# Kernel tuning notes

Measured on AMD Instinct MI355X. Metric: run time of the kernel, lower is better.

Reference implementation:

```python
import jax, jax.numpy as jnp
import numpy as np

CHUNK_LEN = 32
N_HEAD = 32
HEAD_SIZE = 64
EPS = 1e-5 * 64.0  # GroupNorm eps = 1e-5 * head_size_divisor**2
PREC_MIN = 0.005   # rwkv_inner precision_min_val clamp for fp32


def rwkv_inner(r, k, v, w, u, kv_state, chunk_len):
    # r,k,v,w: [B,H,L,K]; u: [H,K]; kv_state: [B,H,K,V]
    B, H, L, K = k.shape
    T = chunk_len
    N = L // T
    w = jnp.clip(w, PREC_MIN, None)
    wc_log = jnp.log(w).reshape(B, H, N, T, K)
    wc_cum = jnp.cumsum(wc_log, axis=-2)                      # [B,H,N,T,K]
    shifted = jnp.concatenate([jnp.zeros_like(wc_cum[..., :1, :]), wc_cum[..., :-1, :]], axis=-2)
    ws_log = jnp.sum(wc_log, axis=-2, keepdims=True)          # [B,H,N,1,K]
    w_inter = jnp.exp(ws_log - wc_cum)                        # decay to end of chunk
    w_intra = jnp.exp(wc_cum - wc_log)                        # decay from start of chunk
    rc = r.reshape(B, H, N, T, K)
    kc = k.reshape(B, H, N, T, K)
    vc = v.reshape(B, H, N, T, K)
    # intra-chunk attention, log-space offset at T//2 for numerical stability
    off = shifted[..., T // 2:T // 2 + 1, :]
    r_decay = jnp.exp(shifted - off)
    k_inv_decay = jnp.exp(off - wc_cum)
    a = jnp.einsum('bhntk,bhnsk->bhnts', rc * r_decay, kc * k_inv_decay)
    a = jnp.tril(a, -1)
    diag = jnp.einsum('bhntk,bhntk->bhnt', rc, u[None, :, None, None, :] * kc)
    out = jnp.einsum('bhnts,bhnsv->bhntv', a, vc) + diag[..., None] * vc
    # per-chunk (k*w_inter)^T @ v contributions, then sequential state carry
    wkv = jnp.einsum('bhntk,bhntv->bhnkv', kc * w_inter, vc)  # [B,H,N,K,V]
    ws = jnp.exp(ws_log)[:, :, :, 0, :]                       # [B,H,N,K]

    def step(state, xs):
        ws_i, wkv_i = xs
        new_state = state * ws_i[..., None] + wkv_i
        return new_state, state

    final_state, states = jax.lax.scan(step, kv_state, (jnp.moveaxis(ws, 2, 0), jnp.moveaxis(wkv, 2, 0)))
    states = jnp.moveaxis(states, 0, 2)                       # [B,H,N,K,V]
    out = out + jnp.einsum('bhntk,bhnkv->bhntv', rc * w_intra, states)
    return out.reshape(B, H, L, K), final_state


def _forward(x, shift_state, wkv_state,
             time_maa_x, time_maa_w, time_maa_k, time_maa_v, time_maa_r, time_maa_g,
             time_maa_w1, time_maa_w2, time_decay, time_decay_w1, time_decay_w2,
             time_faaaa, Wr, Wk, Wv, Wg, Wo, gn_w, gn_b):
    B, T, C = x.shape
    H, K = N_HEAD, HEAD_SIZE
    xprev = jnp.concatenate([shift_state[:, None, :], x[:, :-1]], axis=1)
    dx = xprev - x
    # token-shift LoRA mixing
    xxx = jnp.tanh((x + dx * time_maa_x) @ time_maa_w1).reshape(B, T, 5, -1)
    m = jnp.einsum('btfe,fec->fbtc', xxx, time_maa_w2)  # [5,B,T,C]
    mw, mk, mv, mr, mg = m[0], m[1], m[2], m[3], m[4]
    xk = x + dx * (time_maa_k + mk)
    xv = x + dx * (time_maa_v + mv)
    xr = x + dx * (time_maa_r + mr)
    xg = x + dx * (time_maa_g + mg)
    xw = x + dx * (time_maa_w + mw)
    r = (xr @ Wr.T).reshape(B, T, H, K).transpose(0, 2, 1, 3)
    k = (xk @ Wk.T).reshape(B, T, H, K).transpose(0, 2, 1, 3)
    v = (xv @ Wv.T).reshape(B, T, H, K).transpose(0, 2, 1, 3)
    g = jax.nn.silu(xg @ Wg.T)
    w = time_decay.reshape(1, H, 1, K) + (jnp.tanh(xw @ time_decay_w1) @ time_decay_w2).reshape(B, T, H, K).transpose(0, 2, 1, 3)
    w = jnp.exp(-jnp.exp(w))
    out, wkv_out = rwkv_inner(r, k, v, w, time_faaaa, wkv_state, CHUNK_LEN)
    out = out.transpose(0, 2, 1, 3).reshape(B, T, C)
    # GroupNorm with H groups of K channels
    og = out.reshape(B, T, H, K)
    mu = og.mean(-1, keepdims=True)
    var = og.var(-1, keepdims=True)
    og = (og - mu) * jax.lax.rsqrt(var + EPS)
    out = og.reshape(B, T, C) * gn_w + gn_b
    out = (out * g) @ Wo.T
    return out, x[:, -1], wkv_out


def setup_inputs() -> dict:
    B, T, C = 4, 2048, 2048
    H, K = N_HEAD, HEAD_SIZE
    E5, TD = 32, 64
    key = jax.random.key(0)
    ks = jax.random.split(key, 24)
    f32 = jnp.float32
    inp = {
        'x': jax.random.normal(ks[0], (B, T, C), f32),
        'shift_state': jax.random.normal(ks[1], (B, C), f32),
        'wkv_state': jax.random.normal(ks[2], (B, H, K, K), f32) * 0.1,
        'time_maa_x': jax.random.uniform(ks[3], (1, 1, C), f32),
        'time_maa_w': jax.random.uniform(ks[4], (1, 1, C), f32),
        'time_maa_k': jax.random.uniform(ks[5], (1, 1, C), f32),
        'time_maa_v': jax.random.uniform(ks[6], (1, 1, C), f32),
        'time_maa_r': jax.random.uniform(ks[7], (1, 1, C), f32),
        'time_maa_g': jax.random.uniform(ks[8], (1, 1, C), f32),
        'time_maa_w1': jax.random.uniform(ks[9], (C, E5 * 5), f32, -1e-4, 1e-4),
        'time_maa_w2': jax.random.normal(ks[10], (5, E5, C), f32) * 0.01,
        'time_decay': jnp.linspace(-6.0, -1.0, C, dtype=f32).reshape(1, 1, C),
        'time_decay_w1': jax.random.uniform(ks[11], (C, TD), f32, -1e-4, 1e-4),
        'time_decay_w2': jax.random.normal(ks[12], (TD, C), f32) * 0.01,
        'time_faaaa': jax.random.normal(ks[13], (H, K), f32) * 0.1,
        'Wr': jax.random.normal(ks[14], (C, C), f32) * 0.02,
        'Wk': jax.random.normal(ks[15], (C, C), f32) * 0.02,
        'Wv': jax.random.normal(ks[16], (C, C), f32) * 0.02,
        'Wg': jax.random.normal(ks[17], (C, C), f32) * 0.02,
        'Wo': jax.random.normal(ks[18], (C, C), f32) * 0.02,
        'gn_w': jnp.ones((C,), f32),
        'gn_b': jnp.zeros((C,), f32),
    }
    return inp


def reference(x, shift_state, wkv_state,
              time_maa_x, time_maa_w, time_maa_k, time_maa_v, time_maa_r, time_maa_g,
              time_maa_w1, time_maa_w2, time_decay, time_decay_w1, time_decay_w2,
              time_faaaa, Wr, Wk, Wv, Wg, Wo, gn_w, gn_b):
    return _forward(x, shift_state, wkv_state,
                    time_maa_x, time_maa_w, time_maa_k, time_maa_v, time_maa_r, time_maa_g,
                    time_maa_w1, time_maa_w2, time_decay, time_decay_w1, time_decay_w2,
                    time_faaaa, Wr, Wk, Wv, Wg, Wo, gn_w, gn_b)
```

## Files before the change

kernel.cpp:

```cpp
#include <hip/hip_runtime.h>
#include <stdint.h>
#include <math.h>


typedef __attribute__((ext_vector_type(8))) short bf16x8;
typedef __attribute__((ext_vector_type(4))) float f32x4;

#define AS1(p) ((const __attribute__((address_space(1))) void*)(p))
#define AS3(p) ((__attribute__((address_space(3))) void*)(p))

__device__ __forceinline__ unsigned short f2bf(float f) {
  unsigned int u = __builtin_bit_cast(unsigned int, f);
  u += 0x7fffu + ((u >> 16) & 1u);
  return (unsigned short)(u >> 16);
}
__device__ __forceinline__ float bf2f(unsigned short s) {
  unsigned int u = ((unsigned int)s) << 16;
  return __builtin_bit_cast(float, u);
}
__device__ __forceinline__ unsigned int packbf(float lo, float hi) {
  return (unsigned int)f2bf(lo) | ((unsigned int)f2bf(hi) << 16);
}

template <int EPI, bool BOUNDS>
__global__ __launch_bounds__(256) void gemm_nt(
    const unsigned short* __restrict__ A, const unsigned short* __restrict__ B,
    void* __restrict__ Cp, int M, int N, int K, const float* __restrict__ evec,
    int slot)
{
  __shared__ __align__(16) unsigned short As[128 * 32];
  __shared__ __align__(16) unsigned short Bs[128 * 32];
  const int tid = threadIdx.x;
  const int l = tid & 63, w = tid >> 6;
  const int wm = w & 1, wn = w >> 1;
  const int lm = l & 15, quad = l >> 4;
  const long mBase = (long)blockIdx.y * 128;
  const long nBase = (long)blockIdx.x * 128;

  f32x4 acc[4][4];
  f32x4 zero = {0.f, 0.f, 0.f, 0.f};
#pragma unroll
  for (int i = 0; i < 4; i++)
#pragma unroll
    for (int j = 0; j < 4; j++) acc[i][j] = zero;

  for (int k0 = 0; k0 < K; k0 += 32) {
    if (!BOUNDS) {
      const int r0 = w * 32;
      const int lr = l >> 2, lc = l & 3;
      const unsigned short* gA = A + (mBase + r0 + lr) * (long)K + k0 + lc * 8;
      __builtin_amdgcn_global_load_lds(AS1(gA), AS3(&As[r0 * 32]), 16, 0, 0);
      const unsigned short* gA2 = gA + 16 * (long)K;
      __builtin_amdgcn_global_load_lds(AS1(gA2), AS3(&As[(r0 + 16) * 32]), 16, 0, 0);
      const unsigned short* gB = B + (nBase + r0 + lr) * (long)K + k0 + lc * 8;
      __builtin_amdgcn_global_load_lds(AS1(gB), AS3(&Bs[r0 * 32]), 16, 0, 0);
      const unsigned short* gB2 = gB + 16 * (long)K;
      __builtin_amdgcn_global_load_lds(AS1(gB2), AS3(&Bs[(r0 + 16) * 32]), 16, 0, 0);
    } else {
      const int row = tid >> 2, ch = tid & 3;
#pragma unroll
      for (int rr = 0; rr < 128; rr += 64) {
        int r = rr + row;
        *(int4*)&As[r * 32 + ch * 8] =
            *(const int4*)&A[(mBase + r) * (long)K + k0 + ch * 8];
        int4 bv = make_int4(0, 0, 0, 0);
        long nG = nBase + r;
        if (nG < N) bv = *(const int4*)&B[nG * (long)K + k0 + ch * 8];
        *(int4*)&Bs[r * 32 + ch * 8] = bv;
      }
    }
    __syncthreads();
    bf16x8 af[4], bq[4];
#pragma unroll
    for (int i = 0; i < 4; i++)
      af[i] = *(const bf16x8*)&As[(wm * 64 + i * 16 + lm) * 32 + quad * 8];
#pragma unroll
    for (int i = 0; i < 4; i++)
      bq[i] = *(const bf16x8*)&Bs[(wn * 64 + i * 16 + lm) * 32 + quad * 8];
#pragma unroll
    for (int mi = 0; mi < 4; mi++)
#pragma unroll
      for (int ni = 0; ni < 4; ni++)
        acc[mi][ni] = __builtin_amdgcn_mfma_f32_16x16x32_bf16(af[mi], bq[ni], acc[mi][ni], 0, 0, 0);
    __syncthreads();
  }

#pragma unroll
  for (int mi = 0; mi < 4; mi++) {
#pragma unroll
    for (int ni = 0; ni < 4; ni++) {
      long col = nBase + wn * 64 + ni * 16 + lm;
      if (BOUNDS && col >= N) continue;
      long rw0 = mBase + wm * 64 + mi * 16 + quad * 4;
#pragma unroll
      for (int r = 0; r < 4; r++) {
        float y = acc[mi][ni][r];
        long row = rw0 + r;
        long off = row * (long)N + col;
        if constexpr (EPI == 0) {
          ((float*)Cp)[off] = y;
        } else if constexpr (EPI == 2) {
          ((unsigned short*)Cp)[off] = f2bf(tanhf(y));
        } else if constexpr (EPI == 3) {
          ((unsigned short*)Cp)[off] = f2bf(y / (1.f + __expf(-y)));
        } else if constexpr (EPI == 4) {
          float wv = evec[col] + y;
          ((_Float16*)Cp)[off] = (_Float16)fmaxf(-__expf(wv), -5.2983174f);
        } else if constexpr (EPI == 5) {
          int b = (int)(row >> 11), t = (int)(row & 2047);
          int n = t >> 5, tt = t & 31;
          int h = (int)(col >> 6), kk = (int)(col & 63);
          long c = ((long)(b * 32 + h)) * 64 + n;
          ((unsigned short*)Cp)[c * 6144 + slot + tt * 64 + kk] = f2bf(y);
        }
      }
    }
  }
}

template <int EPI>
__global__ __launch_bounds__(512, 1) void gemm256_nt(
    const unsigned short* __restrict__ A, const unsigned short* __restrict__ B,
    void* __restrict__ Cp, int M, int N, int K, int slot)
{
  __shared__ __align__(16) unsigned short As2[2][16384];
  __shared__ __align__(16) unsigned short Bs2[2][16384];
  const int tid = threadIdx.x;
  const int l = tid & 63;
  const int w = tid >> 6;
  const int wm = w >> 2, wn = w & 3;
  const int lm = l & 15, quad = l >> 4;
  const long mBase = (long)blockIdx.y * 256;
  const long nBase = (long)blockIdx.x * 256;
  const int NT = K >> 6;

  const int r0 = tid >> 3;
  const int csw = (tid & 7) ^ (r0 & 7);
  const int ldsOff = (tid & ~63) * 8;
  const unsigned short* ga0 = A + (mBase + r0) * (long)K + csw * 8;
  const unsigned short* gb0 = B + (nBase + r0) * (long)K + csw * 8;

  f32x4 acc[8][4];
  f32x4 zero = {0.f, 0.f, 0.f, 0.f};
#pragma unroll
  for (int i = 0; i < 8; i++)
#pragma unroll
    for (int j = 0; j < 4; j++) acc[i][j] = zero;

#define STAGE256(kt_)                                                          \
  {                                                                            \
    const int _b = (kt_) & 1;                                                  \
    const unsigned short* _ga = ga0 + (long)(kt_) * 64;                        \
    const unsigned short* _gb = gb0 + (long)(kt_) * 64;                        \
    __builtin_amdgcn_global_load_lds(AS1(_ga), AS3(&As2[_b][ldsOff]), 16, 0, 0);              \
    __builtin_amdgcn_global_load_lds(AS1(_gb), AS3(&Bs2[_b][ldsOff]), 16, 0, 0);              \
    __builtin_amdgcn_global_load_lds(AS1(_ga + (long)64 * K), AS3(&As2[_b][4096 + ldsOff]), 16, 0, 0);  \
    __builtin_amdgcn_global_load_lds(AS1(_gb + (long)64 * K), AS3(&Bs2[_b][4096 + ldsOff]), 16, 0, 0);  \
    __builtin_amdgcn_global_load_lds(AS1(_ga + (long)128 * K), AS3(&As2[_b][8192 + ldsOff]), 16, 0, 0); \
    __builtin_amdgcn_global_load_lds(AS1(_gb + (long)128 * K), AS3(&Bs2[_b][8192 + ldsOff]), 16, 0, 0); \
    __builtin_amdgcn_global_load_lds(AS1(_ga + (long)192 * K), AS3(&As2[_b][12288 + ldsOff]), 16, 0, 0);\
    __builtin_amdgcn_global_load_lds(AS1(_gb + (long)192 * K), AS3(&Bs2[_b][12288 + ldsOff]), 16, 0, 0);\
  }

  STAGE256(0);
  STAGE256(1);
  asm volatile("s_waitcnt vmcnt(8)" ::: "memory");
  __builtin_amdgcn_s_barrier();

  const int q0 = (quad ^ (lm & 7)) * 8;
  const int rA = (wm * 128 + lm) * 64;
  const int rB = (wn * 64 + lm) * 64;

  for (int kt = 0; kt < NT; ++kt) {
    const int b = kt & 1;
    bf16x8 af[8][2], bq[4][2];
#pragma unroll
    for (int fm = 0; fm < 8; fm++)
      af[fm][0] = *(const bf16x8*)&As2[b][rA + fm * 1024 + q0];
#pragma unroll
    for (int fn = 0; fn < 4; fn++)
      bq[fn][0] = *(const bf16x8*)&Bs2[b][rB + fn * 1024 + q0];
#pragma unroll
    for (int fm = 0; fm < 8; fm++)
      af[fm][1] = *(const bf16x8*)&As2[b][rA + fm * 1024 + (q0 ^ 32)];
#pragma unroll
    for (int fn = 0; fn < 4; fn++)
      bq[fn][1] = *(const bf16x8*)&Bs2[b][rB + fn * 1024 + (q0 ^ 32)];

    __builtin_amdgcn_s_setprio(1);
#pragma unroll
    for (int fm = 0; fm < 8; fm++)
#pragma unroll
      for (int fn = 0; fn < 4; fn++)
        acc[fm][fn] = __builtin_amdgcn_mfma_f32_16x16x32_bf16(af[fm][0], bq[fn][0], acc[fm][fn], 0, 0, 0);
    __builtin_amdgcn_s_setprio(0);

    asm volatile("s_waitcnt lgkmcnt(0)" ::: "memory");
    __builtin_amdgcn_s_barrier();
    if (kt + 2 < NT) STAGE256(kt + 2);

    __builtin_amdgcn_s_setprio(1);
#pragma unroll
    for (int fm = 0; fm < 8; fm++)
#pragma unroll
      for (int fn = 0; fn < 4; fn++)
        acc[fm][fn] = __builtin_amdgcn_mfma_f32_16x16x32_bf16(af[fm][1], bq[fn][1], acc[fm][fn], 0, 0, 0);
    __builtin_amdgcn_s_setprio(0);

    if (kt + 2 < NT) {
      asm volatile("s_waitcnt vmcnt(8)" ::: "memory");
    } else {
      asm volatile("s_waitcnt vmcnt(0)" ::: "memory");
    }
    __builtin_amdgcn_s_barrier();
  }
#undef STAGE256

#pragma unroll
  for (int mi = 0; mi < 8; mi++) {
#pragma unroll
    for (int ni = 0; ni < 4; ni++) {
      long col = nBase + wn * 64 + ni * 16 + lm;
      long rw0 = mBase + wm * 128 + mi * 16 + quad * 4;
#pragma unroll
      for (int r = 0; r < 4; r++) {
        float y = acc[mi][ni][r];
        long row = rw0 + r;
        long off = row * (long)N + col;
        if constexpr (EPI == 0) {
          ((float*)Cp)[off] = y;
        } else if constexpr (EPI == 3) {
          ((unsigned short*)Cp)[off] = f2bf(y / (1.f + __expf(-y)));
        } else if constexpr (EPI == 5) {
          int bb = (int)(row >> 11), t = (int)(row & 2047);
          int n = t >> 5, tt = t & 31;
          int h = (int)(col >> 6), kk = (int)(col & 63);
          long c = ((long)(bb * 32 + h)) * 64 + n;
          ((unsigned short*)Cp)[c * 6144 + slot + tt * 64 + kk] = f2bf(y);
        }
      }
    }
  }
}

__global__ __launch_bounds__(256) void k_convert(const float* __restrict__ s,
                                                 unsigned short* __restrict__ d, int n4)
{
  int i = blockIdx.x * 256 + threadIdx.x;
  if (i >= n4) return;
  float4 v = ((const float4*)s)[i];
  short4 o;
  o.x = (short)f2bf(v.x); o.y = (short)f2bf(v.y);
  o.z = (short)f2bf(v.z); o.w = (short)f2bf(v.w);
  ((short4*)d)[i] = o;
}

__global__ __launch_bounds__(256) void k_transpose(const float* __restrict__ s,
                                                   unsigned short* __restrict__ d, int R, int C)
{
  int i = blockIdx.x * 256 + threadIdx.x;
  if (i >= R * C) return;
  int r = i / C, c = i - r * C;
  d[(long)c * R + r] = f2bf(s[i]);
}

__global__ __launch_bounds__(256) void k_prep(const float* __restrict__ x,
                                              const float* __restrict__ shift,
                                              const float* __restrict__ maax,
                                              unsigned short* __restrict__ xmix,
                                              float* __restrict__ xlast)
{
  int i = blockIdx.x * 256 + threadIdx.x;
  int c4 = (i & 511) * 4;
  long bt = i >> 9;
  int t = (int)(bt & 2047);
  long b = bt >> 11;
  float4 xv = *(const float4*)&x[bt * 2048 + c4];
  float4 xp;
  if (t == 0) xp = *(const float4*)&shift[b * 2048 + c4];
  else        xp = *(const float4*)&x[(bt - 1) * 2048 + c4];
  float4 mx = *(const float4*)&maax[c4];
  short4 o;
  o.x = (short)f2bf(xv.x + (xp.x - xv.x) * mx.x);
  o.y = (short)f2bf(xv.y + (xp.y - xv.y) * mx.y);
  o.z = (short)f2bf(xv.z + (xp.z - xv.z) * mx.z);
  o.w = (short)f2bf(xv.w + (xp.w - xv.w) * mx.w);
  *(short4*)&xmix[bt * 2048 + c4] = o;
  if (t == 2047) *(float4*)&xlast[b * 2048 + c4] = xv;
}

__global__ __launch_bounds__(256) void k_mix1(
    const unsigned short* __restrict__ xxx, const unsigned short* __restrict__ w2t,
    const float* __restrict__ x, const float* __restrict__ shift,
    const float* __restrict__ maa, unsigned short* __restrict__ xout, int f)
{
  __shared__ __align__(16) unsigned short As[128 * 32];
  __shared__ __align__(16) unsigned short Bs[128 * 32];
  const int tid = threadIdx.x;
  const int l = tid & 63, w = tid >> 6;
  const int wm = w & 1, wn = w >> 1;
  const int lm = l & 15, quad = l >> 4;
  const long mBase = (long)blockIdx.y * 128;
  const long nBase = (long)blockIdx.x * 128;
  const int row = tid >> 2, ch = tid & 3;
#pragma unroll
  for (int rr = 0; rr < 128; rr += 64) {
    int r = rr + row;
    *(int4*)&As[r * 32 + ch * 8] =
        *(const int4*)&xxx[(mBase + r) * 160 + f * 32 + ch * 8];
    *(int4*)&Bs[r * 32 + ch * 8] =
        *(const int4*)&w2t[((long)f * 2048 + nBase + r) * 32 + ch * 8];
  }
  __syncthreads();
  f32x4 zero = {0.f, 0.f, 0.f, 0.f};
  f32x4 acc[4][4];
#pragma unroll
  for (int i = 0; i < 4; i++)
#pragma unroll
    for (int j = 0; j < 4; j++) acc[i][j] = zero;
  bf16x8 af[4], bq[4];
#pragma unroll
  for (int i = 0; i < 4; i++)
    af[i] = *(const bf16x8*)&As[(wm * 64 + i * 16 + lm) * 32 + quad * 8];
#pragma unroll
  for (int i = 0; i < 4; i++)
    bq[i] = *(const bf16x8*)&Bs[(wn * 64 + i * 16 + lm) * 32 + quad * 8];
#pragma unroll
  for (int mi = 0; mi < 4; mi++)
#pragma unroll
    for (int ni = 0; ni < 4; ni++)
      acc[mi][ni] = __builtin_amdgcn_mfma_f32_16x16x32_bf16(af[mi], bq[ni], acc[mi][ni], 0, 0, 0);

#pragma unroll
  for (int mi = 0; mi < 4; mi++) {
#pragma unroll
    for (int ni = 0; ni < 4; ni++) {
      long col = nBase + wn * 64 + ni * 16 + lm;
#pragma unroll
      for (int r = 0; r < 4; r++) {
        long rg = mBase + wm * 64 + mi * 16 + quad * 4 + r;
        int t = (int)(rg & 2047);
        long b = rg >> 11;
        float xval = x[rg * 2048 + col];
        float xp = t ? x[(rg - 1) * 2048 + col] : shift[b * 2048 + col];
        float res = xval + (xp - xval) * (maa[col] + acc[mi][ni][r]);
        xout[rg * 2048 + col] = f2bf(res);
      }
    }
  }
}

__global__ __launch_bounds__(256) void k_chunk(
    unsigned short* __restrict__ recs, const _Float16* __restrict__ wl,
    const float* __restrict__ u, float* __restrict__ outw,
    float* __restrict__ wsb)
{
  const int chunk = blockIdx.x;
  const int n = chunk & 63, bh = chunk >> 6;
  const int h = bh & 31, b = bh >> 5;
  const int tid = threadIdx.x;
  const int lane = tid & 63, w = tid >> 6;
  const int lm = lane & 15, quad = lane >> 4;
  const long rec = (long)chunk * 6144;
  const long tbase = ((long)(b * 2048 + n * 32)) * 2048 + h * 64;

  __shared__ float rdec[32][68];
  __shared__ float kdec[32][68];
  __shared__ float ssum[4][64];
  __shared__ float offr[64];
  __shared__ float diagr[32];
  __shared__ __align__(16) unsigned short amatH[32][40];
  __shared__ __align__(16) unsigned short amatL[32][40];
  __shared__ __align__(16) unsigned short vcT[64][40];
  __shared__ __align__(16) unsigned short kwH[64][40];
  __shared__ __align__(16) unsigned short kwL[64][40];

  float rv[8], kv[8], wlog[8], cum[8];
#pragma unroll
  for (int j = 0; j < 8; j++) {
    int t = w * 8 + j;
    long g = rec + t * 64 + lane;
    rv[j] = bf2f(recs[g]);
    kv[j] = bf2f(recs[g + 2048]);
    wlog[j] = (float)wl[tbase + (long)t * 2048 + lane];
  }
  {
    float run = 0.f;
#pragma unroll
    for (int j = 0; j < 8; j++) { run += wlog[j]; cum[j] = run; }
    ssum[w][lane] = run;
  }
#pragma unroll
  for (int jp = 0; jp < 4; jp++) {
    int t0 = w * 8 + jp * 2;
    float v0 = bf2f(recs[rec + (t0) * 64 + lane + 4096]);
    float v1 = bf2f(recs[rec + (t0 + 1) * 64 + lane + 4096]);
    *(unsigned int*)&vcT[lane][t0] = packbf(v0, v1);
  }
  __syncthreads();

  float off = 0.f, tot = 0.f;
#pragma unroll
  for (int w2 = 0; w2 < 4; w2++) {
    float s2 = ssum[w2][lane];
    tot += s2;
    if (w2 < w) off += s2;
  }
#pragma unroll
  for (int j = 0; j < 8; j++) cum[j] += off;
  if (w == 1) offr[lane] = cum[7];
  if (w == 0) wsb[(long)chunk * 64 + lane] = __expf(tot);
  __syncthreads();

  const float offv = offr[lane];
  const float uval = u[h * 64 + lane];
#pragma unroll
  for (int jp = 0; jp < 4; jp++) {
    unsigned short h2[2], l2[2];
#pragma unroll
    for (int p = 0; p < 2; p++) {
      int j = jp * 2 + p;
      int t = w * 8 + j;
      float cw = cum[j];
      float sh = cw - wlog[j];
      rdec[t][lane] = rv[j] * __expf(sh - offv);
      kdec[t][lane] = kv[j] * __expf(offv - cw);
      float kw_ = kv[j] * __expf(tot - cw);
      h2[p] = f2bf(kw_);
      l2[p] = f2bf(kw_ - bf2f(h2[p]));
      recs[rec + 4096 + t * 64 + lane] = f2bf(rv[j] * __expf(sh));
    }
    *(unsigned int*)&kwH[lane][w * 8 + jp * 2] = (unsigned int)h2[0] | ((unsigned int)h2[1] << 16);
    *(unsigned int*)&kwL[lane][w * 8 + jp * 2] = (unsigned int)l2[0] | ((unsigned int)l2[1] << 16);
  }
#pragma unroll
  for (int j = 0; j < 8; j++) {
    float d = rv[j] * uval * kv[j];
#pragma unroll
    for (int m = 32; m; m >>= 1) d += __shfl_xor(d, m, 64);
    if (lane == 0) diagr[w * 8 + j] = d;
  }
  __syncthreads();

  {
    const int t0 = (tid >> 4) * 2;
    const int sA = tid & 15;
    float a00 = 0, a01 = 0, a10 = 0, a11 = 0;
#pragma unroll
    for (int kk = 0; kk < 64; kk += 4) {
      float4 r0 = *(const float4*)&rdec[t0][kk];
      float4 r1 = *(const float4*)&rdec[t0 + 1][kk];
      float4 c0 = *(const float4*)&kdec[sA][kk];
      float4 c1 = *(const float4*)&kdec[sA + 16][kk];
      a00 += r0.x * c0.x + r0.y * c0.y + r0.z * c0.z + r0.w * c0.w;
      a01 += r0.x * c1.x + r0.y * c1.y + r0.z * c1.z + r0.w * c1.w;
      a10 += r1.x * c0.x + r1.y * c0.y + r1.z * c0.z + r1.w * c0.w;
      a11 += r1.x * c1.x + r1.y * c1.y + r1.z * c1.z + r1.w * c1.w;
    }
    const int sB = sA + 16;
    float m00 = sA < t0 ? a00 : (sA == t0 ? diagr[t0] : 0.f);
    float m01 = sB < t0 ? a01 : (sB == t0 ? diagr[t0] : 0.f);
    float m10 = sA < t0 + 1 ? a10 : (sA == t0 + 1 ? diagr[t0 + 1] : 0.f);
    float m11 = sB < t0 + 1 ? a11 : (sB == t0 + 1 ? diagr[t0 + 1] : 0.f);
    unsigned short h00 = f2bf(m00), h01 = f2bf(m01), h10 = f2bf(m10), h11 = f2bf(m11);
    amatH[t0][sA] = h00;     amatL[t0][sA] = f2bf(m00 - bf2f(h00));
    amatH[t0][sB] = h01;     amatL[t0][sB] = f2bf(m01 - bf2f(h01));
    amatH[t0 + 1][sA] = h10; amatL[t0 + 1][sA] = f2bf(m10 - bf2f(h10));
    amatH[t0 + 1][sB] = h11; amatL[t0 + 1][sB] = f2bf(m11 - bf2f(h11));
  }
  __syncthreads();

  {
    bf16x8 bv[4];
#pragma unroll
    for (int ni = 0; ni < 4; ni++)
      bv[ni] = *(const bf16x8*)&vcT[ni * 16 + lm][quad * 8];

    const int ti = w >> 1;
    bf16x8 avh = *(const bf16x8*)&amatH[ti * 16 + lm][quad * 8];
    bf16x8 avl = *(const bf16x8*)&amatL[ti * 16 + lm][quad * 8];
    bf16x8 akh = *(const bf16x8*)&kwH[w * 16 + lm][quad * 8];
    bf16x8 akl = *(const bf16x8*)&kwL[w * 16 + lm][quad * 8];

    f32x4 zero = {0.f, 0.f, 0.f, 0.f};
    f32x4 oc0 = zero, oc1 = zero;
    const int nA = (w & 1) * 2;
    oc0 = __builtin_amdgcn_mfma_f32_16x16x32_bf16(avh, bv[nA], oc0, 0, 0, 0);
    oc0 = __builtin_amdgcn_mfma_f32_16x16x32_bf16(avl, bv[nA], oc0, 0, 0, 0);
    oc1 = __builtin_amdgcn_mfma_f32_16x16x32_bf16(avh, bv[nA + 1], oc1, 0, 0, 0);
    oc1 = __builtin_amdgcn_mfma_f32_16x16x32_bf16(avl, bv[nA + 1], oc1, 0, 0, 0);
    f32x4 kc[4];
#pragma unroll
    for (int ni = 0; ni < 4; ni++) {
      kc[ni] = zero;
      kc[ni] = __builtin_amdgcn_mfma_f32_16x16x32_bf16(akh, bv[ni], kc[ni], 0, 0, 0);
      kc[ni] = __builtin_amdgcn_mfma_f32_16x16x32_bf16(akl, bv[ni], kc[ni], 0, 0, 0);
    }

#pragma unroll
    for (int r = 0; r < 4; r++) {
      int t = ti * 16 + quad * 4 + r;
      outw[tbase + (long)t * 2048 + nA * 16 + lm] = oc0[r];
      outw[tbase + (long)t * 2048 + (nA + 1) * 16 + lm] = oc1[r];
    }
#pragma unroll
    for (int ni = 0; ni < 4; ni++)
#pragma unroll
      for (int r = 0; r < 4; r++) {
        int kk = w * 16 + quad * 4 + r;
        recs[rec + kk * 64 + ni * 16 + lm] = f2bf(kc[ni][r]);
      }
  }
}

__global__ __launch_bounds__(256) void k_scan(unsigned short* __restrict__ recs,
                                              const float* __restrict__ wsb,
                                              const float* __restrict__ kv0,
                                              float* __restrict__ finalst)
{
  const int bh = blockIdx.x >> 2;
  const int kq = blockIdx.x & 3;
  const int tid = threadIdx.x;
  float st[4];
  const long base = (long)bh * 4096 + kq * 1024;
#pragma unroll
  for (int j = 0; j < 4; j++) st[j] = kv0[base + j * 256 + tid];
  for (int n = 0; n < 64; n++) {
    const long cb = ((long)bh * 64 + n) * 6144 + kq * 1024;
    const long wb = ((long)bh * 64 + n) * 64 + kq * 16;
#pragma unroll
    for (int j = 0; j < 4; j++) {
      int i = j * 256 + tid;
      unsigned short* p = &recs[cb + i];
      float wv = bf2f(*p);
      *p = f2bf(st[j]);
      st[j] = st[j] * wsb[wb + (i >> 6)] + wv;
    }
  }
#pragma unroll
  for (int j = 0; j < 4; j++) finalst[base + j * 256 + tid] = st[j];
}

__global__ __launch_bounds__(256) void k_inter(const unsigned short* __restrict__ recs,
                                               float* __restrict__ outw)
{
  const int chunk = blockIdx.x;
  const int n = chunk & 63, bh = chunk >> 6;
  const int h = bh & 31, b = bh >> 5;
  const int tid = threadIdx.x;
  const int lane = tid & 63, w = tid >> 6;
  const int lm = lane & 15, quad = lane >> 4;
  const long rec = (long)chunk * 6144;
  const long tbase = ((long)(b * 2048 + n * 32)) * 2048 + h * 64;

  __shared__ __align__(16) unsigned short stT[64][72];
  __shared__ __align__(16) unsigned short rwb[32][72];

  {
    int4 rwv = *(const int4*)&recs[rec + 4096 + tid * 8];
    *(int4*)&rwb[tid >> 3][(tid & 7) * 8] = rwv;
  }
  for (int ii = tid; ii < 4096; ii += 256)
    stT[ii & 63][ii >> 6] = recs[rec + ii];
  __syncthreads();

  const int mi = w >> 1, nset = w & 1;
  bf16x8 aA[2], bB[2][2];
#pragma unroll
  for (int kk = 0; kk < 2; kk++) {
    aA[kk] = *(const bf16x8*)&rwb[mi * 16 + lm][kk * 32 + quad * 8];
#pragma unroll
    for (int p = 0; p < 2; p++)
      bB[p][kk] = *(const bf16x8*)&stT[(nset * 2 + p) * 16 + lm][kk * 32 + quad * 8];
  }
  f32x4 zero = {0.f, 0.f, 0.f, 0.f};
  f32x4 oc[2] = {zero, zero};
#pragma unroll
  for (int kk = 0; kk < 2; kk++) {
    oc[0] = __builtin_amdgcn_mfma_f32_16x16x32_bf16(aA[kk], bB[0][kk], oc[0], 0, 0, 0);
    oc[1] = __builtin_amdgcn_mfma_f32_16x16x32_bf16(aA[kk], bB[1][kk], oc[1], 0, 0, 0);
  }
#pragma unroll
  for (int p = 0; p < 2; p++) {
    int v = (nset * 2 + p) * 16 + lm;
#pragma unroll
    for (int r = 0; r < 4; r++) {
      int t = mi * 16 + quad * 4 + r;
      outw[tbase + (long)t * 2048 + v] += oc[p][r];
    }
  }
}

__global__ __launch_bounds__(256) void k_gnorm(const float* __restrict__ outw,
                                               const unsigned short* __restrict__ gb,
                                               const float* __restrict__ gnw,
                                               const float* __restrict__ gnb,
                                               unsigned short* __restrict__ aout)
{
  const int gid = blockIdx.x * 4 + (threadIdx.x >> 6);
  const int lane = threadIdx.x & 63;
  const long bt = gid >> 5;
  const int h = gid & 31;
  const int c = h * 64 + lane;
  const long off = bt * 2048 + c;
  float y = outw[off];
  float s = y, sq = y * y;
#pragma unroll
  for (int m = 32; m; m >>= 1) {
    s += __shfl_xor(s, m, 64);
    sq += __shfl_xor(sq, m, 64);
  }
  float mu = s * (1.f / 64.f);
  float var = sq * (1.f / 64.f) - mu * mu;
  float nrm = (y - mu) * rsqrtf(var + 6.4e-4f);
  float o = (nrm * gnw[c] + gnb[c]) * bf2f(gb[off]);
  aout[off] = f2bf(o);
}

extern "C" void kernel_launch(void* const* d_in, const int* in_sizes, int n_in,
                              void* d_out, int out_size, void* d_ws, size_t ws_size,
                              hipStream_t stream)
{
  const float* x     = (const float*)d_in[0];
  const float* shift = (const float*)d_in[1];
  const float* kv0   = (const float*)d_in[2];
  const float* maax  = (const float*)d_in[3];
  const float* maaw  = (const float*)d_in[4];
  const float* maak  = (const float*)d_in[5];
  const float* maav  = (const float*)d_in[6];
  const float* maar  = (const float*)d_in[7];
  const float* maag  = (const float*)d_in[8];
  const float* w1    = (const float*)d_in[9];
  const float* w2    = (const float*)d_in[10];
  const float* tdec  = (const float*)d_in[11];
  const float* tdw1  = (const float*)d_in[12];
  const float* tdw2  = (const float*)d_in[13];
  const float* u     = (const float*)d_in[14];
  const float* Wr    = (const float*)d_in[15];
  const float* Wk    = (const float*)d_in[16];
  const float* Wv    = (const float*)d_in[17];
  const float* Wg    = (const float*)d_in[18];
  const float* Wo    = (const float*)d_in[19];
  const float* gnw   = (const float*)d_in[20];
  const float* gnb   = (const float*)d_in[21];

  char* ws = (char*)d_ws;
  const size_t MB = 1048576;
  unsigned short* WbfR  = (unsigned short*)(ws + 0 * MB);
  unsigned short* WbfK  = (unsigned short*)(ws + 8 * MB);
  unsigned short* WbfV  = (unsigned short*)(ws + 16 * MB);
  unsigned short* WbfG  = (unsigned short*)(ws + 24 * MB);
  unsigned short* WbfO  = (unsigned short*)(ws + 32 * MB);
  unsigned short* w2tb  = (unsigned short*)(ws + 40 * MB);
  unsigned short* w1t   = (unsigned short*)(ws + 40 * MB + 655360);
  unsigned short* tdw1t = (unsigned short*)(ws + 40 * MB + 1310720);
  unsigned short* tdw2t = (unsigned short*)(ws + 40 * MB + 1572864);
  unsigned short* xxxb  = (unsigned short*)(ws + 40 * MB + 1835008);
  unsigned short* t1b   = (unsigned short*)(ws + 40 * MB + 4456448);
  float*          wsb   = (float*)(ws + 40 * MB + 5505024);
  unsigned short* xmixb = (unsigned short*)(ws + 48 * MB);
  _Float16*       wlb   = (_Float16*)(ws + 48 * MB);
  unsigned short* x1b   = (unsigned short*)(ws + 80 * MB);
  unsigned short* aob   = (unsigned short*)(ws + 80 * MB);
  unsigned short* recs  = (unsigned short*)(ws + 112 * MB);
  unsigned short* gbuf  = recs;

  float* outp    = (float*)d_out;
  float* xlast   = outp + 16777216;
  float* finalst = outp + 16777216 + 8192;

  k_convert<<<4096, 256, 0, stream>>>(Wr, WbfR, 1048576);
  k_convert<<<4096, 256, 0, stream>>>(Wk, WbfK, 1048576);
  k_convert<<<4096, 256, 0, stream>>>(Wv, WbfV, 1048576);
  k_convert<<<4096, 256, 0, stream>>>(Wg, WbfG, 1048576);
  k_convert<<<4096, 256, 0, stream>>>(Wo, WbfO, 1048576);
  k_transpose<<<1280, 256, 0, stream>>>(w1, w1t, 2048, 160);
  k_transpose<<<512, 256, 0, stream>>>(tdw1, tdw1t, 2048, 64);
  k_transpose<<<512, 256, 0, stream>>>(tdw2, tdw2t, 64, 2048);
  for (int f = 0; f < 5; f++)
    k_transpose<<<256, 256, 0, stream>>>(w2 + (long)f * 65536, w2tb + (long)f * 65536, 32, 2048);

  k_prep<<<16384, 256, 0, stream>>>(x, shift, maax, xmixb, xlast);
  gemm_nt<2, true><<<dim3(2, 64), 256, 0, stream>>>(xmixb, w1t, xxxb, 8192, 160, 2048, nullptr, 0);

  k_mix1<<<dim3(16, 64), 256, 0, stream>>>(xxxb, w2tb, x, shift, maaw, x1b, 0);
  gemm_nt<2, true><<<dim3(1, 64), 256, 0, stream>>>(x1b, tdw1t, t1b, 8192, 64, 2048, nullptr, 0);
  gemm_nt<4, false><<<dim3(16, 64), 256, 0, stream>>>(t1b, tdw2t, wlb, 8192, 2048, 64, tdec, 0);
  k_mix1<<<dim3(16, 64), 256, 0, stream>>>(xxxb, w2tb, x, shift, maak, x1b, 1);
  gemm256_nt<5><<<dim3(8, 32), 512, 0, stream>>>(x1b, WbfK, recs, 8192, 2048, 2048, 2048);
  k_mix1<<<dim3(16, 64), 256, 0, stream>>>(xxxb, w2tb, x, shift, maav, x1b, 2);
  gemm256_nt<5><<<dim3(8, 32), 512, 0, stream>>>(x1b, WbfV, recs, 8192, 2048, 2048, 4096);
  k_mix1<<<dim3(16, 64), 256, 0, stream>>>(xxxb, w2tb, x, shift, maar, x1b, 3);
  gemm256_nt<5><<<dim3(8, 32), 512, 0, stream>>>(x1b, WbfR, recs, 8192, 2048, 2048, 0);
  k_mix1<<<dim3(16, 64), 256, 0, stream>>>(xxxb, w2tb, x, shift, maag, x1b, 4);

  k_chunk<<<8192, 256, 0, stream>>>(recs, wlb, u, outp, wsb);
  k_scan<<<512, 256, 0, stream>>>(recs, wsb, kv0, finalst);
  k_inter<<<8192, 256, 0, stream>>>(recs, outp);

  gemm256_nt<3><<<dim3(8, 32), 512, 0, stream>>>(x1b, WbfG, gbuf, 8192, 2048, 2048, 0);
  k_gnorm<<<65536, 256, 0, stream>>>(outp, gbuf, gnw, gnb, aob);
  gemm256_nt<0><<<dim3(8, 32), 512, 0, stream>>>(aob, WbfO, outp, 8192, 2048, 2048, 0);
}
```

Baseline: 1.240 ms.

## Precompute bf16 x and shift-delta for mix kernels, split scan finer

k_prep now also writes bf16 copies of x and of (x_prev - x) into the not-yet-used output buffer. The five k_mix1 epilogues read these instead of fp32 x plus a conditional shift load, halving their bytes and dropping the branch. k_scan is split into 8 blocks per head instead of 4 for more parallelism, and k_chunk gets a launch-bounds occupancy hint. Rounding x to bf16 before the mix adds a small precision loss.

```diff
diff --git a/kernel.cpp b/kernel.cpp
--- a/kernel.cpp
+++ b/kernel.cpp
@@ -268,7 +268,9 @@
                                               const float* __restrict__ shift,
                                               const float* __restrict__ maax,
                                               unsigned short* __restrict__ xmix,
-                                              float* __restrict__ xlast)
+                                              float* __restrict__ xlast,
+                                              unsigned short* __restrict__ xbf,
+                                              unsigned short* __restrict__ dxbf)
 {
   int i = blockIdx.x * 256 + threadIdx.x;
   int c4 = (i & 511) * 4;
@@ -286,12 +288,20 @@
   o.z = (short)f2bf(xv.z + (xp.z - xv.z) * mx.z);
   o.w = (short)f2bf(xv.w + (xp.w - xv.w) * mx.w);
   *(short4*)&xmix[bt * 2048 + c4] = o;
+  short4 xo;
+  xo.x = (short)f2bf(xv.x); xo.y = (short)f2bf(xv.y);
+  xo.z = (short)f2bf(xv.z); xo.w = (short)f2bf(xv.w);
+  *(short4*)&xbf[bt * 2048 + c4] = xo;
+  short4 dxo;
+  dxo.x = (short)f2bf(xp.x - xv.x); dxo.y = (short)f2bf(xp.y - xv.y);
+  dxo.z = (short)f2bf(xp.z - xv.z); dxo.w = (short)f2bf(xp.w - xv.w);
+  *(short4*)&dxbf[bt * 2048 + c4] = dxo;
   if (t == 2047) *(float4*)&xlast[b * 2048 + c4] = xv;
 }
 
 __global__ __launch_bounds__(256) void k_mix1(
     const unsigned short* __restrict__ xxx, const unsigned short* __restrict__ w2t,
-    const float* __restrict__ x, const float* __restrict__ shift,
+    const unsigned short* __restrict__ xbf, const unsigned short* __restrict__ dxbf,
     const float* __restrict__ maa, unsigned short* __restrict__ xout, int f)
 {
   __shared__ __align__(16) unsigned short As[128 * 32];
@@ -339,18 +349,17 @@
 #pragma unroll
       for (int r = 0; r < 4; r++) {
         long rg = mBase + wm * 64 + mi * 16 + quad * 4 + r;
-        int t = (int)(rg & 2047);
-        long b = rg >> 11;
-        float xval = x[rg * 2048 + col];
-        float xp = t ? x[(rg - 1) * 2048 + col] : shift[b * 2048 + col];
-        float res = xval + (xp - xval) * (maa[col] + acc[mi][ni][r]);
-        xout[rg * 2048 + col] = f2bf(res);
+        long off = rg * 2048 + col;
+        float xval = bf2f(xbf[off]);
+        float dxv = bf2f(dxbf[off]);
+        float res = xval + dxv * (maa[col] + acc[mi][ni][r]);
+        xout[off] = f2bf(res);
       }
     }
   }
 }
 
-__global__ __launch_bounds__(256) void k_chunk(
+__global__ __launch_bounds__(256, 4) void k_chunk(
     unsigned short* __restrict__ recs, const _Float16* __restrict__ wl,
     const float* __restrict__ u, float* __restrict__ outw,
     float* __restrict__ wsb)
@@ -518,18 +527,18 @@
                                               const float* __restrict__ kv0,
                                               float* __restrict__ finalst)
 {
-  const int bh = blockIdx.x >> 2;
-  const int kq = blockIdx.x & 3;
+  const int bh = blockIdx.x >> 3;
+  const int kq = blockIdx.x & 7;
   const int tid = threadIdx.x;
-  float st[4];
-  const long base = (long)bh * 4096 + kq * 1024;
-#pragma unroll
-  for (int j = 0; j < 4; j++) st[j] = kv0[base + j * 256 + tid];
+  float st[2];
+  const long base = (long)bh * 4096 + kq * 512;
+#pragma unroll
+  for (int j = 0; j < 2; j++) st[j] = kv0[base + j * 256 + tid];
   for (int n = 0; n < 64; n++) {
-    const long cb = ((long)bh * 64 + n) * 6144 + kq * 1024;
-    const long wb = ((long)bh * 64 + n) * 64 + kq * 16;
-#pragma unroll
-    for (int j = 0; j < 4; j++) {
+    const long cb = ((long)bh * 64 + n) * 6144 + kq * 512;
+    const long wb = ((long)bh * 64 + n) * 64 + kq * 8;
+#pragma unroll
+    for (int j = 0; j < 2; j++) {
       int i = j * 256 + tid;
       unsigned short* p = &recs[cb + i];
       float wv = bf2f(*p);
@@ -538,7 +547,7 @@
     }
   }
 #pragma unroll
-  for (int j = 0; j < 4; j++) finalst[base + j * 256 + tid] = st[j];
+  for (int j = 0; j < 2; j++) finalst[base + j * 256 + tid] = st[j];
 }
 
 __global__ __launch_bounds__(256) void k_inter(const unsigned short* __restrict__ recs,
@@ -668,6 +677,8 @@
   float* outp    = (float*)d_out;
   float* xlast   = outp + 16777216;
   float* finalst = outp + 16777216 + 8192;
+  unsigned short* xbfb  = (unsigned short*)outp;
+  unsigned short* dxbfb = xbfb + 16777216;
 
   k_convert<<<4096, 256, 0, stream>>>(Wr, WbfR, 1048576);
   k_convert<<<4096, 256, 0, stream>>>(Wk, WbfK, 1048576);
@@ -680,22 +691,22 @@
   for (int f = 0; f < 5; f++)
     k_transpose<<<256, 256, 0, stream>>>(w2 + (long)f * 65536, w2tb + (long)f * 65536, 32, 2048);
 
-  k_prep<<<16384, 256, 0, stream>>>(x, shift, maax, xmixb, xlast);
+  k_prep<<<16384, 256, 0, stream>>>(x, shift, maax, xmixb, xlast, xbfb, dxbfb);
   gemm_nt<2, true><<<dim3(2, 64), 256, 0, stream>>>(xmixb, w1t, xxxb, 8192, 160, 2048, nullptr, 0);
 
-  k_mix1<<<dim3(16, 64), 256, 0, stream>>>(xxxb, w2tb, x, shift, maaw, x1b, 0);
+  k_mix1<<<dim3(16, 64), 256, 0, stream>>>(xxxb, w2tb, xbfb, dxbfb, maaw, x1b, 0);
   gemm_nt<2, true><<<dim3(1, 64), 256, 0, stream>>>(x1b, tdw1t, t1b, 8192, 64, 2048, nullptr, 0);
   gemm_nt<4, false><<<dim3(16, 64), 256, 0, stream>>>(t1b, tdw2t, wlb, 8192, 2048, 64, tdec, 0);
-  k_mix1<<<dim3(16, 64), 256, 0, stream>>>(xxxb, w2tb, x, shift, maak, x1b, 1);
+  k_mix1<<<dim3(16, 64), 256, 0, stream>>>(xxxb, w2tb, xbfb, dxbfb, maak, x1b, 1);
   gemm256_nt<5><<<dim3(8, 32), 512, 0, stream>>>(x1b, WbfK, recs, 8192, 2048, 2048, 2048);
-  k_mix1<<<dim3(16, 64), 256, 0, stream>>>(xxxb, w2tb, x, shift, maav, x1b, 2);
+  k_mix1<<<dim3(16, 64), 256, 0, stream>>>(xxxb, w2tb, xbfb, dxbfb, maav, x1b, 2);
   gemm256_nt<5><<<dim3(8, 32), 512, 0, stream>>>(x1b, WbfV, recs, 8192, 2048, 2048, 4096);
-  k_mix1<<<dim3(16, 64), 256, 0, stream>>>(xxxb, w2tb, x, shift, maar, x1b, 3);
+  k_mix1<<<dim3(16, 64), 256, 0, stream>>>(xxxb, w2tb, xbfb, dxbfb, maar, x1b, 3);
   gemm256_nt<5><<<dim3(8, 32), 512, 0, stream>>>(x1b, WbfR, recs, 8192, 2048, 2048, 0);
-  k_mix1<<<dim3(16, 64), 256, 0, stream>>>(xxxb, w2tb, x, shift, maag, x1b, 4);
+  k_mix1<<<dim3(16, 64), 256, 0, stream>>>(xxxb, w2tb, xbfb, dxbfb, maag, x1b, 4);
 
   k_chunk<<<8192, 256, 0, stream>>>(recs, wlb, u, outp, wsb);
-  k_scan<<<512, 256, 0, stream>>>(recs, wsb, kv0, finalst);
+  k_scan<<<1024, 256, 0, stream>>>(recs, wsb, kv0, finalst);
   k_inter<<<8192, 256, 0, stream>>>(recs, outp);
 
   gemm256_nt<3><<<dim3(8, 32), 512, 0, stream>>>(x1b, WbfG, gbuf, 8192, 2048, 2048, 0);
```

Result: slower. 1.494 ms (+20.5%).
